# Optimization experiments

Hardware: AMD Instinct MI355X
Metric: run time of the kernel (lower is better)

The kernel has to match this reference:

```python
import jax, jax.numpy as jnp
import numpy as np


def setup_inputs() -> dict:
    key = jax.random.key(0)
    kq, kk, kv = jax.random.split(key, 3)
    B, L, S, H, E = 2, 2048, 2048, 8, 64
    queries = jax.random.normal(kq, (B, L, H, E), dtype=jnp.float32)
    keys = jax.random.normal(kk, (B, S, H, E), dtype=jnp.float32)
    values = jax.random.normal(kv, (B, S, H, E), dtype=jnp.float32)
    a1 = jnp.float32(1.0)
    a2 = jnp.float32(1.0)
    return {"queries": queries, "keys": keys, "values": values, "a1": a1, "a2": a2}


def reference(queries, keys, values, a1, a2):
    # queries: (B,L,H,E); keys/values: (B,S,H,E)
    E = queries.shape[-1]
    scale = 1.0 / jnp.sqrt(jnp.float32(E))
    # shared QK scores: (B,H,L,S)
    qk = jnp.einsum('blhe,bshe->bhls', queries, keys) * scale
    # sparse branch: relu^2 (dropout = identity in eval)
    ssa = jnp.square(jax.nn.relu(qk))
    ssa_out = jnp.einsum('bhls,bshd->blhd', ssa, values)
    # dense branch: softmax over keys
    dsa = jax.nn.softmax(qk, axis=-1)
    dsa_out = jnp.einsum('bhls,bshd->blhd', dsa, values)
    w1 = jnp.exp(a1)
    w2 = jnp.exp(a2)
    alpha1 = w1 / (w1 + w2)
    alpha2 = w2 / (w1 + w2)
    return alpha1 * ssa_out + alpha2 * dsa_out
```

## Files before the change

### kernel.cpp

```cpp
#include <hip/hip_runtime.h>

typedef short short4v __attribute__((ext_vector_type(4)));
typedef short short8v __attribute__((ext_vector_type(8)));
typedef float float4v __attribute__((ext_vector_type(4)));
typedef unsigned short u16;

#define NB 2
#define NL 2048
#define NS 2048
#define NH 8
#define NE 64
#define HE (NH*NE)
#define NLT (NL/64)
#define NST (NS/64)
#define TILE_U16 4096

static __device__ __forceinline__ unsigned pk2bf(float a, float b) {
  union { float f; unsigned u; } x, y; x.f = a; y.f = b;
  return __builtin_amdgcn_perm(y.u + 0x8000u, x.u + 0x8000u, 0x07060302u);
}

#define GLD16(gp, lp) __builtin_amdgcn_global_load_lds( \
    (const __attribute__((address_space(1))) void*)(gp), \
    (__attribute__((address_space(3))) void*)(lp), 16, 0, 0)

__global__ __launch_bounds__(256)
void prepack(const float* __restrict__ kp, const float* __restrict__ vp,
             u16* __restrict__ kimg, u16* __restrict__ vimg)
{
  __shared__ __align__(16) u16 ldsv[TILE_U16];

  const int tile = blockIdx.x;
  const int st = tile & (NST - 1);
  const int bh = tile >> 5;
  const int h  = bh & (NH - 1);
  const int b  = bh >> 3;
  const int s0 = st * 64;
  const size_t base = (size_t)b * NS * HE + h * NE;
  const int tid  = threadIdx.x;
  const int wv   = tid >> 6;
  const int lane = tid & 63;
  const int ln7  = lane & 7;

  u16* kt = kimg + (size_t)tile * TILE_U16;
  u16* vt = vimg + (size_t)tile * TILE_U16;

  for (int slot = tid; slot < 512; slot += 256) {
    const int srow = slot >> 3, p = slot & 7, c = p ^ (srow & 7);
    const float* src = kp + base + (size_t)(s0 + srow) * HE + c * 8;
    float4 x0 = *(const float4*)src;
    float4 x1 = *(const float4*)(src + 4);
    unsigned d[4] = { pk2bf(x0.x, x0.y), pk2bf(x0.z, x0.w),
                      pk2bf(x1.x, x1.y), pk2bf(x1.z, x1.w) };
    *(int4*)(kt + slot * 8) = *(const int4*)d;
  }

  {
    const float* vcol = vp + base + (size_t)(s0 + wv * 16) * HE + lane;
    unsigned vr[8];
    #pragma unroll
    for (int jj = 0; jj < 8; ++jj)
      vr[jj] = pk2bf(vcol[(size_t)(2 * jj) * HE], vcol[(size_t)(2 * jj + 1) * HE]);
    #pragma unroll
    for (int i = 0; i < 2; ++i) {
      const int cs = (2 * wv + i) ^ ln7;
      int4 t4 = make_int4((int)vr[4*i+0], (int)vr[4*i+1],
                          (int)vr[4*i+2], (int)vr[4*i+3]);
      *(int4*)(&ldsv[lane * 64 + cs * 8]) = t4;
    }
  }
  __syncthreads();
  {
    const int4* s = (const int4*)ldsv;
    int4* dst = (int4*)vt;
    dst[tid]       = s[tid];
    dst[tid + 256] = s[tid + 256];
  }
}

__global__ __launch_bounds__(256, 2)
void assa_fwd(const float* __restrict__ qp, const u16* __restrict__ kimg,
              const u16* __restrict__ vimg, const float* __restrict__ a1p,
              const float* __restrict__ a2p, float* __restrict__ op)
{
  __shared__ __align__(16) u16 ldsb[2][2 * TILE_U16];

  const int tid  = threadIdx.x;
  const int wv   = tid >> 6;
  const int lane = tid & 63;
  const int ln15 = lane & 15;
  const int ln7  = lane & 7;
  const int quad = lane >> 4;

  const int bid = blockIdx.x;
  const int bh  = bid & 15;
  const int lt  = bid >> 4;
  const int h   = bh & (NH - 1);
  const int b   = bh >> 3;

  const int lbase = lt * 64 + wv * 16;

  short8v qf0, qf1;
  {
    const float* qrow = qp + ((size_t)(b * NL + lbase + ln15)) * HE + h * NE + quad * 8;
    float4 q0 = *(const float4*)(qrow);
    float4 q1 = *(const float4*)(qrow + 4);
    float4 q2 = *(const float4*)(qrow + 32);
    float4 q3 = *(const float4*)(qrow + 36);
    unsigned d0[4] = { pk2bf(0.125f*q0.x, 0.125f*q0.y), pk2bf(0.125f*q0.z, 0.125f*q0.w),
                       pk2bf(0.125f*q1.x, 0.125f*q1.y), pk2bf(0.125f*q1.z, 0.125f*q1.w) };
    unsigned d1[4] = { pk2bf(0.125f*q2.x, 0.125f*q2.y), pk2bf(0.125f*q2.z, 0.125f*q2.w),
                       pk2bf(0.125f*q3.x, 0.125f*q3.y), pk2bf(0.125f*q3.z, 0.125f*q3.w) };
    qf0 = *(const short8v*)d0;
    qf1 = *(const short8v*)d1;
  }

  const size_t tbase = (size_t)bh * NST;

  float4v acc_s[4], acc_d[4];
  #pragma unroll
  for (int t = 0; t < 4; ++t)
    #pragma unroll
    for (int r = 0; r < 4; ++r) { acc_s[t][r] = 0.0f; acc_d[t][r] = 0.0f; }

  float l_part = 0.0f;

  auto dma_tile = [&](int st, int nb) {
    const int half = wv & 1;
    const u16* g;
    u16* l;
    if (wv < 2) {
      g = kimg + (tbase + st) * TILE_U16 + half * 2048 + lane * 8;
      l = &ldsb[nb][half * 2048];
    } else {
      g = vimg + (tbase + st) * TILE_U16 + half * 2048 + lane * 8;
      l = &ldsb[nb][TILE_U16 + half * 2048];
    }
    GLD16(g,        l);
    GLD16(g +  512, l +  512);
    GLD16(g + 1024, l + 1024);
    GLD16(g + 1536, l + 1536);
  };

  dma_tile(0, 0);

  for (int st = 0; st < NST; ++st) {
    __builtin_amdgcn_s_waitcnt(0);
    __syncthreads();
    if (st + 1 < NST) dma_tile(st + 1, (st + 1) & 1);

    const u16* kb_l = ldsb[st & 1];
    const u16* vb_l = ldsb[st & 1] + TILE_U16;

    #pragma unroll
    for (int u = 0; u < 4; ++u) {
      float4v sa; sa[0] = 0.0f; sa[1] = 0.0f; sa[2] = 0.0f; sa[3] = 0.0f;
      short8v kf0 = *(const short8v*)(&kb_l[(u * 16 + ln15) * 64 + ((quad ^ ln7) * 8)]);
      short8v kf1 = *(const short8v*)(&kb_l[(u * 16 + ln15) * 64 + (((4 + quad) ^ ln7) * 8)]);
      sa = __builtin_amdgcn_mfma_f32_16x16x32_bf16(kf0, qf0, sa, 0, 0, 0);
      sa = __builtin_amdgcn_mfma_f32_16x16x32_bf16(kf1, qf1, sa, 0, 0, 0);

      float ps[4], pd[4];
      #pragma unroll
      for (int r = 0; r < 4; ++r) {
        float sc = sa[r];
        float rl = sc > 0.0f ? sc : 0.0f;
        ps[r] = rl * rl;
        pd[r] = __expf(sc);
        l_part += pd[r];
      }
      unsigned da[2] = { pk2bf(ps[0], ps[1]), pk2bf(ps[2], ps[3]) };
      unsigned db[2] = { pk2bf(pd[0], pd[1]), pk2bf(pd[2], pd[3]) };
      short4v as = *(const short4v*)da;
      short4v ad = *(const short4v*)db;
      #pragma unroll
      for (int t = 0; t < 4; ++t) {
        short4v vf = *(const short4v*)(&vb_l[(t * 16 + ln15) * 64 +
                        (((2 * u + (quad >> 1)) ^ ln7) * 8) + (quad & 1) * 4]);
        acc_s[t] = __builtin_amdgcn_mfma_f32_16x16x16bf16_1k(as, vf, acc_s[t], 0, 0, 0);
        acc_d[t] = __builtin_amdgcn_mfma_f32_16x16x16bf16_1k(ad, vf, acc_d[t], 0, 0, 0);
      }
    }
  }

  l_part += __shfl_xor(l_part, 16, 64);
  l_part += __shfl_xor(l_part, 32, 64);

  const float w1 = __expf(a1p[0]), w2 = __expf(a2p[0]);
  const float al1 = w1 / (w1 + w2);
  const float al2 = w2 / (w1 + w2);

  float c_d[4];
  #pragma unroll
  for (int r = 0; r < 4; ++r) {
    float ls = __shfl(l_part, quad * 4 + r, 64);
    c_d[r] = al2 / ls;
  }

  #pragma unroll
  for (int t = 0; t < 4; ++t) {
    #pragma unroll
    for (int r = 0; r < 4; ++r) {
      float val = al1 * acc_s[t][r] + c_d[r] * acc_d[t][r];
      const int l = lbase + quad * 4 + r;
      const int e = t * 16 + ln15;
      op[((size_t)(b * NL + l)) * HE + h * NE + e] = val;
    }
  }
}

extern "C" void kernel_launch(void* const* d_in, const int* in_sizes, int n_in,
                              void* d_out, int out_size, void* d_ws, size_t ws_size,
                              hipStream_t stream) {
  const float* q  = (const float*)d_in[0];
  const float* k  = (const float*)d_in[1];
  const float* v  = (const float*)d_in[2];
  const float* a1 = (const float*)d_in[3];
  const float* a2 = (const float*)d_in[4];
  float* out = (float*)d_out;
  (void)in_sizes; (void)n_in; (void)out_size; (void)ws_size;

  u16* kimg = (u16*)d_ws;
  u16* vimg = kimg + (size_t)NB * NH * NST * TILE_U16;

  prepack<<<dim3(NB * NH * NST), dim3(256), 0, stream>>>(k, v, kimg, vimg);
  assa_fwd<<<dim3(NB * NH * NLT), dim3(256), 0, stream>>>(q, kimg, vimg, a1, a2, out);
}
```

Before: 117.2 us.

## Use 16x16x32 MFMA for PV by permuting key rows and swizzle

Processes two 16-key score blocks together and permutes which K rows each lane computes. That lets the P·V product use the K=32 bf16 MFMA with 8-element operands instead of the K=16 variant, which halves the number of PV MFMA instructions and widens V LDS reads to 16 bytes. The K prepack swizzle changes to match the new row permutation so LDS reads stay free of bank conflicts. The cost is higher register pressure from the extra score fragments, and correctness depends on the permuted row and swizzle mapping being exactly right.

```diff
diff --git a/kernel.cpp b/kernel.cpp
--- a/kernel.cpp
+++ b/kernel.cpp
@@ -23,6 +23,8 @@
 #define GLD16(gp, lp) __builtin_amdgcn_global_load_lds( \
     (const __attribute__((address_space(1))) void*)(gp), \
     (__attribute__((address_space(3))) void*)(lp), 16, 0, 0)
+
+static __device__ __forceinline__ int fK(int s) { return (s & 3) | ((s >> 1) & 4); }
 
 __global__ __launch_bounds__(256)
 void prepack(const float* __restrict__ kp, const float* __restrict__ vp,
@@ -46,7 +48,7 @@
   u16* vt = vimg + (size_t)tile * TILE_U16;
 
   for (int slot = tid; slot < 512; slot += 256) {
-    const int srow = slot >> 3, p = slot & 7, c = p ^ (srow & 7);
+    const int srow = slot >> 3, p = slot & 7, c = p ^ fK(srow);
     const float* src = kp + base + (size_t)(s0 + srow) * HE + c * 8;
     float4 x0 = *(const float4*)src;
     float4 x1 = *(const float4*)(src + 4);
@@ -144,6 +146,9 @@
 
   dma_tile(0, 0);
 
+  const int rperm = 8 * (ln15 >> 2) + (ln15 & 3);
+  const int fk    = (ln15 & 3) | (((ln15 >> 2) & 1) << 2);
+
   for (int st = 0; st < NST; ++st) {
     __builtin_amdgcn_s_waitcnt(0);
     __syncthreads();
@@ -153,32 +158,44 @@
     const u16* vb_l = ldsb[st & 1] + TILE_U16;
 
     #pragma unroll
-    for (int u = 0; u < 4; ++u) {
-      float4v sa; sa[0] = 0.0f; sa[1] = 0.0f; sa[2] = 0.0f; sa[3] = 0.0f;
-      short8v kf0 = *(const short8v*)(&kb_l[(u * 16 + ln15) * 64 + ((quad ^ ln7) * 8)]);
-      short8v kf1 = *(const short8v*)(&kb_l[(u * 16 + ln15) * 64 + (((4 + quad) ^ ln7) * 8)]);
-      sa = __builtin_amdgcn_mfma_f32_16x16x32_bf16(kf0, qf0, sa, 0, 0, 0);
-      sa = __builtin_amdgcn_mfma_f32_16x16x32_bf16(kf1, qf1, sa, 0, 0, 0);
-
-      float ps[4], pd[4];
+    for (int U = 0; U < 2; ++U) {
+      float4v sa0, sa1;
+      #pragma unroll
+      for (int r = 0; r < 4; ++r) { sa0[r] = 0.0f; sa1[r] = 0.0f; }
+      const u16* krow0 = &kb_l[(32 * U + rperm) * 64];
+      const u16* krow1 = krow0 + 4 * 64;
+      short8v kf00 = *(const short8v*)(krow0 + (quad ^ fk) * 8);
+      short8v kf01 = *(const short8v*)(krow0 + ((4 + quad) ^ fk) * 8);
+      short8v kf10 = *(const short8v*)(krow1 + (quad ^ fk) * 8);
+      short8v kf11 = *(const short8v*)(krow1 + ((4 + quad) ^ fk) * 8);
+      sa0 = __builtin_amdgcn_mfma_f32_16x16x32_bf16(kf00, qf0, sa0, 0, 0, 0);
+      sa0 = __builtin_amdgcn_mfma_f32_16x16x32_bf16(kf01, qf1, sa0, 0, 0, 0);
+      sa1 = __builtin_amdgcn_mfma_f32_16x16x32_bf16(kf10, qf0, sa1, 0, 0, 0);
+      sa1 = __builtin_amdgcn_mfma_f32_16x16x32_bf16(kf11, qf1, sa1, 0, 0, 0);
+
+      float ps[8], pd[8];
       #pragma unroll
       for (int r = 0; r < 4; ++r) {
-        float sc = sa[r];
-        float rl = sc > 0.0f ? sc : 0.0f;
-        ps[r] = rl * rl;
-        pd[r] = __expf(sc);
-        l_part += pd[r];
+        float s0 = sa0[r], s1 = sa1[r];
+        float r0 = s0 > 0.0f ? s0 : 0.0f;
+        float r1 = s1 > 0.0f ? s1 : 0.0f;
+        ps[r] = r0 * r0;  ps[4 + r] = r1 * r1;
+        pd[r] = __expf(s0); pd[4 + r] = __expf(s1);
+        l_part += pd[r] + pd[4 + r];
       }
-      unsigned da[2] = { pk2bf(ps[0], ps[1]), pk2bf(ps[2], ps[3]) };
-      unsigned db[2] = { pk2bf(pd[0], pd[1]), pk2bf(pd[2], pd[3]) };
-      short4v as = *(const short4v*)da;
-      short4v ad = *(const short4v*)db;
+      unsigned da[4] = { pk2bf(ps[0], ps[1]), pk2bf(ps[2], ps[3]),
+                         pk2bf(ps[4], ps[5]), pk2bf(ps[6], ps[7]) };
+      unsigned db[4] = { pk2bf(pd[0], pd[1]), pk2bf(pd[2], pd[3]),
+                         pk2bf(pd[4], pd[5]), pk2bf(pd[6], pd[7]) };
+      short8v as8 = *(const short8v*)da;
+      short8v ad8 = *(const short8v*)db;
+
       #pragma unroll
       for (int t = 0; t < 4; ++t) {
-        short4v vf = *(const short4v*)(&vb_l[(t * 16 + ln15) * 64 +
-                        (((2 * u + (quad >> 1)) ^ ln7) * 8) + (quad & 1) * 4]);
-        acc_s[t] = __builtin_amdgcn_mfma_f32_16x16x16bf16_1k(as, vf, acc_s[t], 0, 0, 0);
-        acc_d[t] = __builtin_amdgcn_mfma_f32_16x16x16bf16_1k(ad, vf, acc_d[t], 0, 0, 0);
+        short8v vf = *(const short8v*)(&vb_l[(t * 16 + ln15) * 64 +
+                        (((4 * U + quad) ^ ln7) * 8)]);
+        acc_s[t] = __builtin_amdgcn_mfma_f32_16x16x32_bf16(as8, vf, acc_s[t], 0, 0, 0);
+        acc_d[t] = __builtin_amdgcn_mfma_f32_16x16x32_bf16(ad8, vf, acc_d[t], 0, 0, 0);
       }
     }
   }
```

Measured after the change: 112.9 us. 1.04x faster.
